# Kernel tuning notes

Hardware: AMD Instinct MI355X
Metric: run time of the kernel (lower is better)

## Reference

```python
import jax, jax.numpy as jnp
import numpy as np

B, N, C = 32, 320, 768
H = 12
LT, LS = 64, 256
HD = C // H
MLP_H = 4 * C
EPS = 1e-5


def _ln(x, g, b):
    m = jnp.mean(x, axis=-1, keepdims=True)
    v = jnp.var(x, axis=-1, keepdims=True)
    return (x - m) * jax.lax.rsqrt(v + EPS) * g + b


def setup_inputs() -> dict:
    key = jax.random.key(0)
    ks = jax.random.split(key, 16)
    s = 0.02
    inp = {
        'x': jax.random.normal(ks[0], (B, N, C), jnp.float32),
        'global_index_template': jax.random.randint(ks[1], (B, LT), 0, LT),
        'global_index_search': jax.random.randint(ks[2], (B, LS), 0, LS),
        'g1': jnp.ones((C,), jnp.float32), 'b1': jnp.zeros((C,), jnp.float32),
        'Wqkv': jax.random.normal(ks[3], (C, 3 * C), jnp.float32) * s,
        'Wproj': jax.random.normal(ks[4], (C, C), jnp.float32) * s,
        'bproj': jnp.zeros((C,), jnp.float32),
        'g2': jnp.ones((C,), jnp.float32), 'b2': jnp.zeros((C,), jnp.float32),
        'W1': jax.random.normal(ks[5], (C, MLP_H), jnp.float32) * s,
        'bm1': jnp.zeros((MLP_H,), jnp.float32),
        'W2': jax.random.normal(ks[6], (MLP_H, C), jnp.float32) * s,
        'bm2': jnp.zeros((C,), jnp.float32),
        'Wg': jax.random.normal(ks[7], (C, C), jnp.float32) * s,
        'bg': jnp.zeros((C,), jnp.float32),
        'g3': jnp.ones((C,), jnp.float32), 'b3': jnp.zeros((C,), jnp.float32),
    }
    return inp


def reference(x, global_index_template, global_index_search, g1, b1, Wqkv, Wproj, bproj,
              g2, b2, W1, bm1, W2, bm2, Wg, bg, g3, b3):
    scale = HD ** (-0.5)
    # --- Attention ---
    xn = _ln(x, g1, b1)
    qkv = (xn @ Wqkv).reshape(B, N, 3, H, HD)
    q, k, v = qkv[:, :, 0], qkv[:, :, 1], qkv[:, :, 2]  # [B,N,H,HD]
    logits = jnp.einsum('bnhd,bmhd->bhnm', q, k) * scale
    attn = jax.nn.softmax(logits, axis=-1)  # [B,H,N,N]
    ctx = jnp.einsum('bhnm,bmhd->bnhd', attn, v).reshape(B, N, C)
    x = x + (ctx @ Wproj + bproj)
    # --- MLP ---
    h = jax.nn.gelu(_ln(x, g2, b2) @ W1 + bm1, approximate=False)
    x = x + (h @ W2 + bm2)
    # --- Block-adjacency from attention (avg pooling) ---
    w_ts = jnp.sum(attn[:, :, :LT, LT:], axis=1) / H  # [B,LT,LS]
    w_ts = jax.nn.softmax(w_ts, axis=2)
    adj = jnp.zeros((B, N, N), x.dtype)
    adj = adj.at[:, :LT, LT:].set(w_ts)
    adj = adj.at[:, LT:, :LT].set(jnp.swapaxes(w_ts, 1, 2))
    # --- GCN layer ---
    support = x @ Wg + bg
    x = jnp.einsum('bnm,bmc->bnc', adj, support)
    x = x + _ln(x, g3, b3)
    return x
```

## Files before the change

kernel.cpp:

```cpp
#include <hip/hip_runtime.h>
#include <stdint.h>

#define NB 32
#define NSEQ 320
#define CDIM 768
#define NH 12
#define HD 64
#define MLPH 3072
#define MROWS (NB*NSEQ)

typedef __attribute__((ext_vector_type(8))) short v8s;
typedef __attribute__((ext_vector_type(4))) float v4f;

__device__ __forceinline__ unsigned short f2b(float f){
  unsigned int u = __float_as_uint(f);
  u += 0x7fffu + ((u >> 16) & 1u);
  return (unsigned short)(u >> 16);
}
__device__ __forceinline__ float b2f(unsigned short h){
  return __uint_as_float(((unsigned int)h) << 16);
}
__device__ __forceinline__ void glds16(const unsigned short* g, unsigned short* l){
  __builtin_amdgcn_global_load_lds(
      (const __attribute__((address_space(1))) void*)g,
      (__attribute__((address_space(3))) void*)l, 16, 0, 0);
}

__global__ __launch_bounds__(256)
void castAll(const float* __restrict__ Wqkv, const float* __restrict__ Wproj,
             const float* __restrict__ W1,   const float* __restrict__ W2,
             const float* __restrict__ Wg,
             unsigned short* __restrict__ wqkvT, unsigned short* __restrict__ wprojT,
             unsigned short* __restrict__ w1T,   unsigned short* __restrict__ w2T,
             unsigned short* __restrict__ wgT){
  int bid = blockIdx.x;
  const float* W; unsigned short* Wt; int K, N, KT;
  if (bid < 1728){ W = Wqkv; Wt = wqkvT; K = 768; N = 2304; KT = 24; }
  else if (bid < 1728+576){ bid -= 1728; W = Wproj; Wt = wprojT; K = 768; N = 768; KT = 24; }
  else if (bid < 1728+576+2304){ bid -= 1728+576; W = W1; Wt = w1T; K = 768; N = 3072; KT = 24; }
  else if (bid < 1728+576+2304+2304){ bid -= 1728+576+2304; W = W2; Wt = w2T; K = 3072; N = 768; KT = 96; }
  else { bid -= 1728+576+2304+2304; W = Wg; Wt = wgT; K = 768; N = 768; KT = 24; }
  const int k0 = (bid % KT) * 32, n0 = (bid / KT) * 32;
  __shared__ float tile[32][33];
  const int tx = threadIdx.x & 31, ty = threadIdx.x >> 5;
  #pragma unroll
  for (int i = 0; i < 32; i += 8)
    tile[ty + i][tx] = W[(size_t)(k0 + ty + i) * N + n0 + tx];
  __syncthreads();
  #pragma unroll
  for (int i = 0; i < 32; i += 8)
    Wt[(size_t)(n0 + ty + i) * K + k0 + tx] = f2b(tile[tx][ty + i]);
}

__global__ __launch_bounds__(192)
void ln_to_bf16(const float* __restrict__ x, const float* __restrict__ g,
                const float* __restrict__ be, unsigned short* __restrict__ out){
  const int row = blockIdx.x;
  const int t = threadIdx.x, w = t >> 6, l = t & 63;
  const float4 v = *(const float4*)(x + (size_t)row * CDIM + t * 4);
  float s  = v.x + v.y + v.z + v.w;
  float s2 = v.x*v.x + v.y*v.y + v.z*v.z + v.w*v.w;
  __shared__ float r1[3], r2[3];
  #pragma unroll
  for (int d = 1; d < 64; d <<= 1){ s += __shfl_xor(s, d, 64); s2 += __shfl_xor(s2, d, 64); }
  if (l == 0){ r1[w] = s; r2[w] = s2; }
  __syncthreads();
  const float S = r1[0] + r1[1] + r1[2];
  const float S2 = r2[0] + r2[1] + r2[2];
  const float mean = S * (1.0f / CDIM);
  const float var  = S2 * (1.0f / CDIM) - mean * mean;
  const float rs = rsqrtf(var + 1e-5f);
  const float4 gg = *(const float4*)(g + t * 4);
  const float4 bb = *(const float4*)(be + t * 4);
  ushort4 o;
  o.x = f2b((v.x - mean) * rs * gg.x + bb.x);
  o.y = f2b((v.y - mean) * rs * gg.y + bb.y);
  o.z = f2b((v.z - mean) * rs * gg.z + bb.z);
  o.w = f2b((v.w - mean) * rs * gg.w + bb.w);
  *(ushort4*)(out + (size_t)row * CDIM + t * 4) = o;
}

template<bool BIAS, bool RES, bool GELU, bool WB, bool WF>
__global__ __launch_bounds__(256, 3)
void gemm_cv(const unsigned short* __restrict__ A, const unsigned short* __restrict__ Bt,
             int N, int K,
             const float* __restrict__ bias, const float* __restrict__ res,
             unsigned short* __restrict__ outb, float* __restrict__ outf){
  __shared__ __align__(16) unsigned short lds[3 * 8192];
  const int tid = threadIdx.x;
  const int w = tid >> 6, l = tid & 63;
  const int bm = blockIdx.x, bn = blockIdx.y;
  const int wr = w >> 1, wc = w & 1;
  const int nkt = K >> 5;
  v4f acc[4][4] = {};

  const int srow = w * 32 + (l >> 2);
  const int scol = (l & 3) * 8;
  const unsigned short* Ag = A + (size_t)(bm * 128 + srow) * K + scol;
  const unsigned short* Bg = Bt + (size_t)(bn * 128 + srow) * K + scol;
  const int ldst = (w * 32) * 32;

  auto stage = [&](int bufi, int kt){
    unsigned short* Ab = lds + bufi * 8192;
    #pragma unroll
    for (int i = 0; i < 2; ++i){
      glds16(Ag + (size_t)(i * 16) * K + kt * 32, Ab + ldst + i * 512);
      glds16(Bg + (size_t)(i * 16) * K + kt * 32, Ab + 4096 + ldst + i * 512);
    }
  };

  auto body = [&](int kt, int cbuf){
    if (kt + 2 < nkt) stage((cbuf + 2) % 3, kt + 2);
    const unsigned short* Ab = lds + cbuf * 8192;
    const unsigned short* Bb = Ab + 4096;
    const int kk = (l >> 4) << 3;
    v8s af[4], bfr[4];
    #pragma unroll
    for (int mi = 0; mi < 4; ++mi)
      af[mi] = *(const v8s*)&Ab[(wr * 64 + mi * 16 + (l & 15)) * 32 + kk];
    #pragma unroll
    for (int ni = 0; ni < 4; ++ni)
      bfr[ni] = *(const v8s*)&Bb[(wc * 64 + ni * 16 + (l & 15)) * 32 + kk];
    __builtin_amdgcn_s_setprio(1);
    #pragma unroll
    for (int mi = 0; mi < 4; ++mi)
      #pragma unroll
      for (int ni = 0; ni < 4; ++ni)
        acc[mi][ni] = __builtin_amdgcn_mfma_f32_16x16x32_bf16(af[mi], bfr[ni], acc[mi][ni], 0, 0, 0);
    __builtin_amdgcn_s_setprio(0);
    if (kt + 2 < nkt)      asm volatile("s_waitcnt vmcnt(4)" ::: "memory");
    else if (kt + 1 < nkt) asm volatile("s_waitcnt vmcnt(0)" ::: "memory");
    if (kt + 1 < nkt) __builtin_amdgcn_s_barrier();
  };

  stage(0, 0); stage(1, 1);
  asm volatile("s_waitcnt vmcnt(4)" ::: "memory");
  __builtin_amdgcn_s_barrier();

  #pragma unroll 1
  for (int base = 0; base < nkt; base += 3){
    body(base + 0, 0);
    body(base + 1, 1);
    body(base + 2, 2);
  }

  const int r0 = bm * 128 + wr * 64 + ((l >> 4) << 2);
  const int c0 = bn * 128 + wc * 64 + (l & 15);
  #pragma unroll
  for (int mi = 0; mi < 4; ++mi){
    #pragma unroll
    for (int rr = 0; rr < 4; ++rr){
      const int row = r0 + mi * 16 + rr;
      #pragma unroll
      for (int ni = 0; ni < 4; ++ni){
        const int col = c0 + ni * 16;
        float c = acc[mi][ni][rr];
        if (BIAS) c += bias[col];
        if (RES)  c += res[(size_t)row * N + col];
        if (GELU) c = 0.5f * c * (1.0f + erff(c * 0.70710678118f));
        if (WB) outb[(size_t)row * N + col] = f2b(c);
        if (WF) outf[(size_t)row * N + col] = c;
      }
    }
  }
}

__global__ __launch_bounds__(256, 2)
void attn_kernel(const unsigned short* __restrict__ qkv,
                 unsigned short* __restrict__ ctx,
                 float* __restrict__ wparts){
  __shared__ __align__(16) unsigned short Qs[64 * 72];
  __shared__ __align__(16) unsigned short KV[64 * 72];
  __shared__ __align__(16) unsigned short Ps[64 * 328];
  const int t = threadIdx.x;
  const int w = t >> 6, l = t & 63;
  const int bid = blockIdx.x;
  const int qt = bid % 5;
  const int h  = (bid / 5) % NH;
  const int b  = bid / (5 * NH);
  const size_t base = (size_t)b * NSEQ * 2304 + h * 64;

  {
    const int r = t >> 3, seg = t & 7;
    #pragma unroll
    for (int i = 0; i < 2; ++i){
      const int r2 = r + 32 * i;
      const unsigned short* src = qkv + base + (size_t)(qt * 64 + r2) * 2304 + seg * 8;
      *(uint4*)&Qs[r2 * 72 + seg * 8] = *(const uint4*)src;
    }
  }
  __syncthreads();
  const int qr = 16 * w + (l & 15);
  const v8s aq0 = *(const v8s*)&Qs[qr * 72 + ((l >> 4) << 3)];
  const v8s aq1 = *(const v8s*)&Qs[qr * 72 + 32 + ((l >> 4) << 3)];

  v4f sacc[20] = {};
  for (int kt = 0; kt < 5; ++kt){
    __syncthreads();
    {
      const int r = t >> 3, seg = t & 7;
      #pragma unroll
      for (int i = 0; i < 2; ++i){
        const int r2 = r + 32 * i;
        const unsigned short* src = qkv + base + 768 + (size_t)(kt * 64 + r2) * 2304 + seg * 8;
        *(uint4*)&KV[r2 * 72 + seg * 8] = *(const uint4*)src;
      }
    }
    __syncthreads();
    #pragma unroll
    for (int f = 0; f < 4; ++f){
      const int kr = 16 * f + (l & 15);
      const v8s b0 = *(const v8s*)&KV[kr * 72 + ((l >> 4) << 3)];
      const v8s b1 = *(const v8s*)&KV[kr * 72 + 32 + ((l >> 4) << 3)];
      sacc[kt * 4 + f] = __builtin_amdgcn_mfma_f32_16x16x32_bf16(aq0, b0, sacc[kt * 4 + f], 0, 0, 0);
      sacc[kt * 4 + f] = __builtin_amdgcn_mfma_f32_16x16x32_bf16(aq1, b1, sacc[kt * 4 + f], 0, 0, 0);
    }
  }

  const float scale = 0.125f;
  #pragma unroll
  for (int r = 0; r < 4; ++r){
    float m = -1e30f;
    #pragma unroll
    for (int f = 0; f < 20; ++f) m = fmaxf(m, sacc[f][r]);
    #pragma unroll
    for (int d = 1; d < 16; d <<= 1) m = fmaxf(m, __shfl_xor(m, d, 64));
    const float Ms = m * scale;
    float sum = 0.f;
    #pragma unroll
    for (int f = 0; f < 20; ++f){ float p = expf(sacc[f][r] * scale - Ms); sacc[f][r] = p; sum += p; }
    #pragma unroll
    for (int d = 1; d < 16; d <<= 1) sum += __shfl_xor(sum, d, 64);
    const float inv = 1.0f / sum;
    const int rowq = 16 * w + ((l >> 4) << 2) + r;
    #pragma unroll
    for (int f = 0; f < 20; ++f)
      Ps[rowq * 328 + f * 16 + (l & 15)] = f2b(sacc[f][r] * inv);
    if (qt == 0){
      #pragma unroll
      for (int f = 4; f < 20; ++f)
        wparts[(((size_t)b * NH + h) * 64 + rowq) * 256 + (f - 4) * 16 + (l & 15)] = sacc[f][r] * inv;
    }
  }

  v4f cacc[4] = {};
  for (int kt = 0; kt < 5; ++kt){
    __syncthreads();
    {
      const int m = t & 31, d0 = (t >> 5) * 8;
      #pragma unroll
      for (int i = 0; i < 2; ++i){
        const int m2 = m + 32 * i;
        const unsigned short* src = qkv + base + 1536 + (size_t)(kt * 64 + m2) * 2304 + d0;
        uint4 dv = *(const uint4*)src;
        const unsigned short* e = (const unsigned short*)&dv;
        #pragma unroll
        for (int jj = 0; jj < 8; ++jj) KV[(d0 + jj) * 72 + m2] = e[jj];
      }
    }
    __syncthreads();
    const int pr = 16 * w + (l & 15);
    const v8s pa0 = *(const v8s*)&Ps[pr * 328 + kt * 64 + ((l >> 4) << 3)];
    const v8s pa1 = *(const v8s*)&Ps[pr * 328 + kt * 64 + 32 + ((l >> 4) << 3)];
    #pragma unroll
    for (int f = 0; f < 4; ++f){
      const int vc = 16 * f + (l & 15);
      const v8s bv0 = *(const v8s*)&KV[vc * 72 + ((l >> 4) << 3)];
      const v8s bv1 = *(const v8s*)&KV[vc * 72 + 32 + ((l >> 4) << 3)];
      cacc[f] = __builtin_amdgcn_mfma_f32_16x16x32_bf16(pa0, bv0, cacc[f], 0, 0, 0);
      cacc[f] = __builtin_amdgcn_mfma_f32_16x16x32_bf16(pa1, bv1, cacc[f], 0, 0, 0);
    }
  }
  #pragma unroll
  for (int f = 0; f < 4; ++f)
    #pragma unroll
    for (int rr = 0; rr < 4; ++rr){
      const int rowq = 16 * w + ((l >> 4) << 2) + rr;
      const int col = 16 * f + (l & 15);
      ctx[(size_t)(b * NSEQ + qt * 64 + rowq) * CDIM + h * 64 + col] = f2b(cacc[f][rr]);
    }
}

__global__ __launch_bounds__(256)
void wts_softmax(const float* __restrict__ wparts,
                 unsigned short* __restrict__ wtsb,
                 unsigned short* __restrict__ wtsbT){
  const int row = blockIdx.x;
  const int b = row >> 6, n = row & 63;
  const int j = threadIdx.x;
  const int w = j >> 6, l = j & 63;
  float s = 0.f;
  #pragma unroll
  for (int hh = 0; hh < NH; ++hh)
    s += wparts[(((size_t)b * NH + hh) * 64 + n) * 256 + j];
  s *= (1.0f / NH);
  __shared__ float red[8];
  float m = s;
  #pragma unroll
  for (int d = 1; d < 64; d <<= 1) m = fmaxf(m, __shfl_xor(m, d, 64));
  if (l == 0) red[w] = m;
  __syncthreads();
  m = fmaxf(fmaxf(red[0], red[1]), fmaxf(red[2], red[3]));
  const float e = expf(s - m);
  float sm = e;
  #pragma unroll
  for (int d = 1; d < 64; d <<= 1) sm += __shfl_xor(sm, d, 64);
  if (l == 0) red[4 + w] = sm;
  __syncthreads();
  const float tot = red[4] + red[5] + red[6] + red[7];
  const unsigned short p = f2b(e / tot);
  wtsb [((size_t)b * 64 + n) * 256 + j] = p;
  wtsbT[((size_t)b * 256 + j) * 64 + n] = p;
}

__global__ __launch_bounds__(256)
void transT(const unsigned short* __restrict__ in, unsigned short* __restrict__ out){
  __shared__ unsigned short tile[64][65];
  const int c0 = blockIdx.x * 64, n0 = blockIdx.y * 64, b = blockIdx.z;
  const int tx = threadIdx.x & 31, ty = threadIdx.x >> 5;
  const unsigned short* ib = in + (size_t)b * NSEQ * CDIM;
  unsigned short* ob = out + (size_t)b * CDIM * NSEQ;
  #pragma unroll
  for (int i = 0; i < 64; i += 8){
    const unsigned int v = *(const unsigned int*)&ib[(size_t)(n0 + ty + i) * CDIM + c0 + tx * 2];
    tile[tx * 2][ty + i]     = (unsigned short)(v & 0xffff);
    tile[tx * 2 + 1][ty + i] = (unsigned short)(v >> 16);
  }
  __syncthreads();
  #pragma unroll
  for (int i = 0; i < 64; i += 8){
    const int c = ty + i;
    const unsigned int v = (unsigned int)tile[c][tx * 2] | ((unsigned int)tile[c][tx * 2 + 1] << 16);
    *(unsigned int*)&ob[(size_t)(c0 + c) * NSEQ + n0 + tx * 2] = v;
  }
}

template<int KC, int SH2>
__global__ __launch_bounds__(256, 2)
void graph_gemm(const unsigned short* __restrict__ A, int KTOT,
                const unsigned short* __restrict__ supT, int koff,
                float* __restrict__ y, int rowoff){
  __shared__ __align__(16) unsigned short As[64 * KC];
  __shared__ __align__(16) unsigned short Bs[128 * KC];
  const int t = threadIdx.x, w = t >> 6, l = t & 63;
  const int mt = blockIdx.x, ct = blockIdx.y, b = blockIdx.z;
  const char* Ab = (const char*)(A + (size_t)b * 16384 + (size_t)mt * 64 * KTOT);
  const char* Bb = (const char*)(supT + (size_t)b * CDIM * NSEQ);
  v4f acc[4][2] = {};

  const int nch = KTOT / KC;
  for (int ch = 0; ch < nch; ++ch){
    if (ch) __syncthreads();
    const int kbase = (koff + ch * KC) * 2;
    #pragma unroll
    for (int i = 0; i < KC / 32; ++i){
      const int gi = w * (KC / 32) + i;
      const int X = gi * 1024 + l * 16;
      const int c = X >> SH2;
      const int k2 = (X & (KC * 2 - 1)) ^ ((c & 7) << 4);
      glds16((const unsigned short*)(Ab + (size_t)c * (KTOT * 2) + ch * KC * 2 + k2),
             As + (gi * 512));
    }
    #pragma unroll
    for (int i = 0; i < KC / 16; ++i){
      const int gi = w * (KC / 16) + i;
      const int X = gi * 1024 + l * 16;
      const int c = X >> SH2;
      const int k2 = (X & (KC * 2 - 1)) ^ ((c & 7) << 4);
      glds16((const unsigned short*)(Bb + (size_t)(ct * 128 + c) * (NSEQ * 2) + kbase + k2),
             Bs + (gi * 512));
    }
    __syncthreads();
    #pragma unroll
    for (int ks = 0; ks < KC / 32; ++ks){
      const int kbyte = ks * 64 + ((l >> 4) << 4);
      v8s af[4], bf2[2];
      #pragma unroll
      for (int mi = 0; mi < 4; ++mi){
        const int r = mi * 16 + (l & 15);
        af[mi] = *(const v8s*)((const char*)As + (r << SH2) + (kbyte ^ ((r & 7) << 4)));
      }
      #pragma unroll
      for (int ni = 0; ni < 2; ++ni){
        const int rb = w * 32 + ni * 16 + (l & 15);
        bf2[ni] = *(const v8s*)((const char*)Bs + (rb << SH2) + (kbyte ^ ((rb & 7) << 4)));
      }
      #pragma unroll
      for (int mi = 0; mi < 4; ++mi)
        #pragma unroll
        for (int ni = 0; ni < 2; ++ni)
          acc[mi][ni] = __builtin_amdgcn_mfma_f32_16x16x32_bf16(af[mi], bf2[ni], acc[mi][ni], 0, 0, 0);
    }
  }

  const int r0 = rowoff + mt * 64 + ((l >> 4) << 2);
  const int c0 = ct * 128 + w * 32 + (l & 15);
  #pragma unroll
  for (int mi = 0; mi < 4; ++mi)
    #pragma unroll
    for (int ni = 0; ni < 2; ++ni)
      #pragma unroll
      for (int rr = 0; rr < 4; ++rr)
        y[((size_t)b * NSEQ + r0 + mi * 16 + rr) * CDIM + c0 + ni * 16] = acc[mi][ni][rr];
}

__global__ __launch_bounds__(192)
void ln_final(const float* __restrict__ y, const float* __restrict__ g3,
              const float* __restrict__ b3, float* __restrict__ out){
  const int row = blockIdx.x;
  const int t = threadIdx.x, w = t >> 6, l = t & 63;
  const float4 v = *(const float4*)(y + (size_t)row * CDIM + t * 4);
  float s  = v.x + v.y + v.z + v.w;
  float s2 = v.x*v.x + v.y*v.y + v.z*v.z + v.w*v.w;
  __shared__ float r1[3], r2[3];
  #pragma unroll
  for (int d = 1; d < 64; d <<= 1){ s += __shfl_xor(s, d, 64); s2 += __shfl_xor(s2, d, 64); }
  if (l == 0){ r1[w] = s; r2[w] = s2; }
  __syncthreads();
  const float S = r1[0] + r1[1] + r1[2];
  const float S2 = r2[0] + r2[1] + r2[2];
  const float mean = S * (1.0f / CDIM);
  const float var  = S2 * (1.0f / CDIM) - mean * mean;
  const float rs = rsqrtf(var + 1e-5f);
  const float4 gg = *(const float4*)(g3 + t * 4);
  const float4 bb = *(const float4*)(b3 + t * 4);
  float4 o;
  o.x = v.x + (v.x - mean) * rs * gg.x + bb.x;
  o.y = v.y + (v.y - mean) * rs * gg.y + bb.y;
  o.z = v.z + (v.z - mean) * rs * gg.z + bb.z;
  o.w = v.w + (v.w - mean) * rs * gg.w + bb.w;
  *(float4*)(out + (size_t)row * CDIM + t * 4) = o;
}

extern "C" void kernel_launch(void* const* d_in, const int* in_sizes, int n_in,
                              void* d_out, int out_size, void* d_ws, size_t ws_size,
                              hipStream_t stream){
  (void)in_sizes; (void)n_in; (void)out_size; (void)ws_size;
  const float* x    = (const float*)d_in[0];
  const float* g1   = (const float*)d_in[3];
  const float* b1   = (const float*)d_in[4];
  const float* Wqkv = (const float*)d_in[5];
  const float* Wproj= (const float*)d_in[6];
  const float* bproj= (const float*)d_in[7];
  const float* g2   = (const float*)d_in[8];
  const float* b2   = (const float*)d_in[9];
  const float* W1   = (const float*)d_in[10];
  const float* bm1  = (const float*)d_in[11];
  const float* W2   = (const float*)d_in[12];
  const float* bm2  = (const float*)d_in[13];
  const float* Wg   = (const float*)d_in[14];
  const float* bg   = (const float*)d_in[15];
  const float* g3   = (const float*)d_in[16];
  const float* b3   = (const float*)d_in[17];
  float* out = (float*)d_out;
  char* ws = (char*)d_ws;

  unsigned short* wqkvT = (unsigned short*)(ws + 0);
  unsigned short* wprojT= (unsigned short*)(ws + 3538944);
  unsigned short* w1T   = (unsigned short*)(ws + 4718592);
  unsigned short* w2T   = (unsigned short*)(ws + 9437184);
  unsigned short* wgT   = (unsigned short*)(ws + 14155776);
  unsigned short* xn1   = (unsigned short*)(ws + 15335424);
  unsigned short* qkvb  = (unsigned short*)(ws + 31064064);
  unsigned short* hb    = (unsigned short*)(ws + 15335424);
  unsigned short* supT  = (unsigned short*)(ws + 15335424);
  unsigned short* ctxb  = (unsigned short*)(ws + 78249984);
  unsigned short* x2b   = (unsigned short*)(ws + 78249984);
  unsigned short* xn2   = (unsigned short*)(ws + 93978624);
  unsigned short* supb  = (unsigned short*)(ws + 93978624);
  float*          x1    = (float*)(ws + 109707264);
  float*          wparts= (float*)(ws + 109707264);
  float*          yb    = (float*)(ws + 109707264);
  unsigned short* wtsb  = (unsigned short*)(ws + 141164544);
  unsigned short* wtsbT = (unsigned short*)(ws + 142213120);

  castAll<<<7488, 256, 0, stream>>>(Wqkv, Wproj, W1, W2, Wg,
                                    wqkvT, wprojT, w1T, w2T, wgT);

  ln_to_bf16<<<MROWS, 192, 0, stream>>>(x, g1, b1, xn1);

  gemm_cv<false,false,false,true,false><<<dim3(80, 18), 256, 0, stream>>>(
      xn1, wqkvT, 2304, CDIM, nullptr, nullptr, qkvb, nullptr);

  attn_kernel<<<NB * NH * 5, 256, 0, stream>>>(qkvb, ctxb, wparts);

  wts_softmax<<<NB * 64, 256, 0, stream>>>(wparts, wtsb, wtsbT);

  gemm_cv<true,true,false,false,true><<<dim3(80, 6), 256, 0, stream>>>(
      ctxb, wprojT, CDIM, CDIM, bproj, x, nullptr, x1);

  ln_to_bf16<<<MROWS, 192, 0, stream>>>(x1, g2, b2, xn2);

  gemm_cv<true,false,true,true,false><<<dim3(80, 24), 256, 0, stream>>>(
      xn2, w1T, MLPH, CDIM, bm1, nullptr, hb, nullptr);

  gemm_cv<true,true,false,true,false><<<dim3(80, 6), 256, 0, stream>>>(
      hb, w2T, CDIM, MLPH, bm2, x1, x2b, nullptr);

  gemm_cv<true,false,false,true,false><<<dim3(80, 6), 256, 0, stream>>>(
      x2b, wgT, CDIM, CDIM, bg, nullptr, supb, nullptr);

  transT<<<dim3(CDIM/64, NSEQ/64, NB), 256, 0, stream>>>(supb, supT);

  graph_gemm<128, 8><<<dim3(1, 6, NB), 256, 0, stream>>>(wtsb, 256, supT, 64, yb, 0);
  graph_gemm<64, 7><<<dim3(4, 6, NB), 256, 0, stream>>>(wtsbT, 64, supT, 0, yb, 64);

  ln_final<<<MROWS, 192, 0, stream>>>(yb, g3, b3, out);
}
```

Baseline: 477.3 us.

## Store residual x1 in bf16 and stream attention probabilities per tile

The post-attention residual x1 is now written and read as bf16 rather than fp32, which halves its traffic in the projection epilogue, the second layernorm and the W2 residual add. The attention kernel no longer keeps the full 64x320 probability matrix in LDS. It holds the normalized probabilities in registers and writes a 64x64 bf16 tile per key block, with row padding changed to 80. The smaller LDS footprint lets the kernel raise its launch bound to 3 blocks per SM. The risk is lower precision in the residual path and an extra LDS write per K/V iteration.

```diff
diff --git a/kernel.cpp b/kernel.cpp
--- a/kernel.cpp
+++ b/kernel.cpp
@@ -52,12 +52,19 @@
     Wt[(size_t)(n0 + ty + i) * K + k0 + tx] = f2b(tile[tx][ty + i]);
 }
 
+template<bool INB16>
 __global__ __launch_bounds__(192)
-void ln_to_bf16(const float* __restrict__ x, const float* __restrict__ g,
+void ln_to_bf16(const void* __restrict__ xin, const float* __restrict__ g,
                 const float* __restrict__ be, unsigned short* __restrict__ out){
   const int row = blockIdx.x;
   const int t = threadIdx.x, w = t >> 6, l = t & 63;
-  const float4 v = *(const float4*)(x + (size_t)row * CDIM + t * 4);
+  float4 v;
+  if (INB16){
+    const ushort4 vb = *(const ushort4*)((const unsigned short*)xin + (size_t)row * CDIM + t * 4);
+    v.x = b2f(vb.x); v.y = b2f(vb.y); v.z = b2f(vb.z); v.w = b2f(vb.w);
+  } else {
+    v = *(const float4*)((const float*)xin + (size_t)row * CDIM + t * 4);
+  }
   float s  = v.x + v.y + v.z + v.w;
   float s2 = v.x*v.x + v.y*v.y + v.z*v.z + v.w*v.w;
   __shared__ float r1[3], r2[3];
@@ -80,11 +87,12 @@
   *(ushort4*)(out + (size_t)row * CDIM + t * 4) = o;
 }
 
-template<bool BIAS, bool RES, bool GELU, bool WB, bool WF>
+template<bool BIAS, bool RES, bool RESB, bool GELU, bool WB, bool WF>
 __global__ __launch_bounds__(256, 3)
 void gemm_cv(const unsigned short* __restrict__ A, const unsigned short* __restrict__ Bt,
              int N, int K,
-             const float* __restrict__ bias, const float* __restrict__ res,
+             const float* __restrict__ bias, const float* __restrict__ resf,
+             const unsigned short* __restrict__ resb,
              unsigned short* __restrict__ outb, float* __restrict__ outf){
   __shared__ __align__(16) unsigned short lds[3 * 8192];
   const int tid = threadIdx.x;
@@ -156,7 +164,7 @@
         const int col = c0 + ni * 16;
         float c = acc[mi][ni][rr];
         if (BIAS) c += bias[col];
-        if (RES)  c += res[(size_t)row * N + col];
+        if (RES)  c += RESB ? b2f(resb[(size_t)row * N + col]) : resf[(size_t)row * N + col];
         if (GELU) c = 0.5f * c * (1.0f + erff(c * 0.70710678118f));
         if (WB) outb[(size_t)row * N + col] = f2b(c);
         if (WF) outf[(size_t)row * N + col] = c;
@@ -165,13 +173,13 @@
   }
 }
 
-__global__ __launch_bounds__(256, 2)
+__global__ __launch_bounds__(256, 3)
 void attn_kernel(const unsigned short* __restrict__ qkv,
                  unsigned short* __restrict__ ctx,
                  float* __restrict__ wparts){
-  __shared__ __align__(16) unsigned short Qs[64 * 72];
-  __shared__ __align__(16) unsigned short KV[64 * 72];
-  __shared__ __align__(16) unsigned short Ps[64 * 328];
+  __shared__ __align__(16) unsigned short Qs[64 * 80];
+  __shared__ __align__(16) unsigned short KV[64 * 80];
+  __shared__ __align__(16) unsigned short Pst[64 * 80];
   const int t = threadIdx.x;
   const int w = t >> 6, l = t & 63;
   const int bid = blockIdx.x;
@@ -179,6 +187,7 @@
   const int h  = (bid / 5) % NH;
   const int b  = bid / (5 * NH);
   const size_t base = (size_t)b * NSEQ * 2304 + h * 64;
+  const int g8 = (l >> 4) << 3;
 
   {
     const int r = t >> 3, seg = t & 7;
@@ -186,13 +195,13 @@
     for (int i = 0; i < 2; ++i){
       const int r2 = r + 32 * i;
       const unsigned short* src = qkv + base + (size_t)(qt * 64 + r2) * 2304 + seg * 8;
-      *(uint4*)&Qs[r2 * 72 + seg * 8] = *(const uint4*)src;
+      *(uint4*)&Qs[r2 * 80 + seg * 8] = *(const uint4*)src;
     }
   }
   __syncthreads();
   const int qr = 16 * w + (l & 15);
-  const v8s aq0 = *(const v8s*)&Qs[qr * 72 + ((l >> 4) << 3)];
-  const v8s aq1 = *(const v8s*)&Qs[qr * 72 + 32 + ((l >> 4) << 3)];
+  const v8s aq0 = *(const v8s*)&Qs[qr * 80 + g8];
+  const v8s aq1 = *(const v8s*)&Qs[qr * 80 + 32 + g8];
 
   v4f sacc[20] = {};
   for (int kt = 0; kt < 5; ++kt){
@@ -203,15 +212,15 @@
       for (int i = 0; i < 2; ++i){
         const int r2 = r + 32 * i;
         const unsigned short* src = qkv + base + 768 + (size_t)(kt * 64 + r2) * 2304 + seg * 8;
-        *(uint4*)&KV[r2 * 72 + seg * 8] = *(const uint4*)src;
+        *(uint4*)&KV[r2 * 80 + seg * 8] = *(const uint4*)src;
       }
     }
     __syncthreads();
     #pragma unroll
     for (int f = 0; f < 4; ++f){
       const int kr = 16 * f + (l & 15);
-      const v8s b0 = *(const v8s*)&KV[kr * 72 + ((l >> 4) << 3)];
-      const v8s b1 = *(const v8s*)&KV[kr * 72 + 32 + ((l >> 4) << 3)];
+      const v8s b0 = *(const v8s*)&KV[kr * 80 + g8];
+      const v8s b1 = *(const v8s*)&KV[kr * 80 + 32 + g8];
       sacc[kt * 4 + f] = __builtin_amdgcn_mfma_f32_16x16x32_bf16(aq0, b0, sacc[kt * 4 + f], 0, 0, 0);
       sacc[kt * 4 + f] = __builtin_amdgcn_mfma_f32_16x16x32_bf16(aq1, b1, sacc[kt * 4 + f], 0, 0, 0);
     }
@@ -232,14 +241,13 @@
     #pragma unroll
     for (int d = 1; d < 16; d <<= 1) sum += __shfl_xor(sum, d, 64);
     const float inv = 1.0f / sum;
-    const int rowq = 16 * w + ((l >> 4) << 2) + r;
-    #pragma unroll
-    for (int f = 0; f < 20; ++f)
-      Ps[rowq * 328 + f * 16 + (l & 15)] = f2b(sacc[f][r] * inv);
+    #pragma unroll
+    for (int f = 0; f < 20; ++f) sacc[f][r] *= inv;
     if (qt == 0){
+      const int rowq = 16 * w + ((l >> 4) << 2) + r;
       #pragma unroll
       for (int f = 4; f < 20; ++f)
-        wparts[(((size_t)b * NH + h) * 64 + rowq) * 256 + (f - 4) * 16 + (l & 15)] = sacc[f][r] * inv;
+        wparts[(((size_t)b * NH + h) * 64 + rowq) * 256 + (f - 4) * 16 + (l & 15)] = sacc[f][r];
     }
   }
 
@@ -255,18 +263,27 @@
         uint4 dv = *(const uint4*)src;
         const unsigned short* e = (const unsigned short*)&dv;
         #pragma unroll
-        for (int jj = 0; jj < 8; ++jj) KV[(d0 + jj) * 72 + m2] = e[jj];
+        for (int jj = 0; jj < 8; ++jj) KV[(d0 + jj) * 80 + m2] = e[jj];
+      }
+    }
+    {
+      #pragma unroll
+      for (int r = 0; r < 4; ++r){
+        const int rowq = 16 * w + ((l >> 4) << 2) + r;
+        #pragma unroll
+        for (int fp = 0; fp < 4; ++fp)
+          Pst[rowq * 80 + fp * 16 + (l & 15)] = f2b(sacc[kt * 4 + fp][r]);
       }
     }
     __syncthreads();
     const int pr = 16 * w + (l & 15);
-    const v8s pa0 = *(const v8s*)&Ps[pr * 328 + kt * 64 + ((l >> 4) << 3)];
-    const v8s pa1 = *(const v8s*)&Ps[pr * 328 + kt * 64 + 32 + ((l >> 4) << 3)];
+    const v8s pa0 = *(const v8s*)&Pst[pr * 80 + g8];
+    const v8s pa1 = *(const v8s*)&Pst[pr * 80 + 32 + g8];
     #pragma unroll
     for (int f = 0; f < 4; ++f){
       const int vc = 16 * f + (l & 15);
-      const v8s bv0 = *(const v8s*)&KV[vc * 72 + ((l >> 4) << 3)];
-      const v8s bv1 = *(const v8s*)&KV[vc * 72 + 32 + ((l >> 4) << 3)];
+      const v8s bv0 = *(const v8s*)&KV[vc * 80 + g8];
+      const v8s bv1 = *(const v8s*)&KV[vc * 80 + 32 + g8];
       cacc[f] = __builtin_amdgcn_mfma_f32_16x16x32_bf16(pa0, bv0, cacc[f], 0, 0, 0);
       cacc[f] = __builtin_amdgcn_mfma_f32_16x16x32_bf16(pa1, bv1, cacc[f], 0, 0, 0);
     }
@@ -468,7 +485,7 @@
   unsigned short* x2b   = (unsigned short*)(ws + 78249984);
   unsigned short* xn2   = (unsigned short*)(ws + 93978624);
   unsigned short* supb  = (unsigned short*)(ws + 93978624);
-  float*          x1    = (float*)(ws + 109707264);
+  unsigned short* x1b   = (unsigned short*)(ws + 109707264);
   float*          wparts= (float*)(ws + 109707264);
   float*          yb    = (float*)(ws + 109707264);
   unsigned short* wtsb  = (unsigned short*)(ws + 141164544);
@@ -477,28 +494,28 @@
   castAll<<<7488, 256, 0, stream>>>(Wqkv, Wproj, W1, W2, Wg,
                                     wqkvT, wprojT, w1T, w2T, wgT);
 
-  ln_to_bf16<<<MROWS, 192, 0, stream>>>(x, g1, b1, xn1);
-
-  gemm_cv<false,false,false,true,false><<<dim3(80, 18), 256, 0, stream>>>(
-      xn1, wqkvT, 2304, CDIM, nullptr, nullptr, qkvb, nullptr);
+  ln_to_bf16<false><<<MROWS, 192, 0, stream>>>(x, g1, b1, xn1);
+
+  gemm_cv<false,false,false,false,true,false><<<dim3(80, 18), 256, 0, stream>>>(
+      xn1, wqkvT, 2304, CDIM, nullptr, nullptr, nullptr, qkvb, nullptr);
 
   attn_kernel<<<NB * NH * 5, 256, 0, stream>>>(qkvb, ctxb, wparts);
 
   wts_softmax<<<NB * 64, 256, 0, stream>>>(wparts, wtsb, wtsbT);
 
-  gemm_cv<true,true,false,false,true><<<dim3(80, 6), 256, 0, stream>>>(
-      ctxb, wprojT, CDIM, CDIM, bproj, x, nullptr, x1);
-
-  ln_to_bf16<<<MROWS, 192, 0, stream>>>(x1, g2, b2, xn2);
-
-  gemm_cv<true,false,true,true,false><<<dim3(80, 24), 256, 0, stream>>>(
-      xn2, w1T, MLPH, CDIM, bm1, nullptr, hb, nullptr);
-
-  gemm_cv<true,true,false,true,false><<<dim3(80, 6), 256, 0, stream>>>(
-      hb, w2T, CDIM, MLPH, bm2, x1, x2b, nullptr);
-
-  gemm_cv<true,false,false,true,false><<<dim3(80, 6), 256, 0, stream>>>(
-      x2b, wgT, CDIM, CDIM, bg, nullptr, supb, nullptr);
+  gemm_cv<true,true,false,false,true,false><<<dim3(80, 6), 256, 0, stream>>>(
+      ctxb, wprojT, CDIM, CDIM, bproj, x, nullptr, x1b, nullptr);
+
+  ln_to_bf16<true><<<MROWS, 192, 0, stream>>>(x1b, g2, b2, xn2);
+
+  gemm_cv<true,false,false,true,true,false><<<dim3(80, 24), 256, 0, stream>>>(
+      xn2, w1T, MLPH, CDIM, bm1, nullptr, nullptr, hb, nullptr);
+
+  gemm_cv<true,true,true,false,true,false><<<dim3(80, 6), 256, 0, stream>>>(
+      hb, w2T, CDIM, MLPH, bm2, nullptr, x1b, x2b, nullptr);
+
+  gemm_cv<true,false,false,false,true,false><<<dim3(80, 6), 256, 0, stream>>>(
+      x2b, wgT, CDIM, CDIM, bg, nullptr, nullptr, supb, nullptr);
 
   transT<<<dim3(CDIM/64, NSEQ/64, NB), 256, 0, stream>>>(supb, supT);
 
```

New measurement: 518.0 us. 8.5% more time.
